# Performance work log

Hardware: AMD Instinct MI355X
Metric: run time of the kernel (lower is better)

The kernel has to match this reference:

```python
import jax, jax.numpy as jnp
import numpy as np

N_NODES = 50000
N_EDGES = 800000
D_IN = 512
D_OUT = 256

def setup_inputs() -> dict:
    key = jax.random.key(0)
    k1, k2, k3, k4, k5 = jax.random.split(key, 5)
    return {
        "inputs": jax.random.normal(k1, (N_NODES, D_IN), dtype=jnp.float32),
        "weights": jax.random.uniform(k2, (D_IN, D_OUT), dtype=jnp.float32, minval=-0.1, maxval=0.1),
        "bias": jnp.zeros((D_OUT,), dtype=jnp.float32),
        "edge_vals": jax.random.uniform(k3, (N_EDGES,), dtype=jnp.float32),
        "edge_row": jax.random.randint(k4, (N_EDGES,), 0, N_NODES),
        "edge_col": jax.random.randint(k5, (N_EDGES,), 0, N_NODES),
    }

def reference(inputs, weights, bias, edge_vals, edge_row, edge_col):
    # dense projection: [N, D_in] @ [D_in, D_out] -> [N, D_out]
    supports = inputs @ weights
    # sparse adjacency spmm in COO form: out[i] = sum_e vals[e] * supports[col[e]] for row[e] == i
    msgs = supports[edge_col] * edge_vals[:, None]  # [E, D_out]
    aggregated = jax.ops.segment_sum(msgs, edge_row, num_segments=inputs.shape[0])
    return aggregated + bias
```

## Files before the change

### kernel.cpp

```cpp
#include <hip/hip_runtime.h>

#define D_IN 512
#define D_OUT 256
#define BM 128
#define BN 128
#define BK 32
#define LDK 40

typedef short short8 __attribute__((ext_vector_type(8)));
typedef float floatx4 __attribute__((ext_vector_type(4)));

static __device__ __forceinline__ unsigned short f2bf(float f) {
    unsigned u = __float_as_uint(f);
    u += 0x7FFF + ((u >> 16) & 1);
    return (unsigned short)(u >> 16);
}
static __device__ __forceinline__ float bf2f(unsigned short h) {
    return __uint_as_float((unsigned)h << 16);
}

__global__ __launch_bounds__(256) void convert_w(const float* __restrict__ W,
                                                 unsigned short* __restrict__ Wt) {
    int t = blockIdx.x * 256 + threadIdx.x;
    int n = t >> 9;
    int k = t & 511;
    Wt[t] = f2bf(W[(size_t)k * D_OUT + n]);
}

__global__ __launch_bounds__(512) void gemm_bf16(const float* __restrict__ A,
                                                 const unsigned short* __restrict__ Wt,
                                                 unsigned short* __restrict__ S, int M) {
    __shared__ unsigned short As[BM * LDK];
    __shared__ unsigned short Bs[BN * LDK];
    const int tid  = threadIdx.x;
    const int lane = tid & 63;
    const int wave = tid >> 6;
    const int wm   = (wave >> 2) * 64;
    const int wn   = (wave & 3) * 32;
    const int bm   = blockIdx.x * BM;
    const int bn   = blockIdx.y * BN;
    const int l15  = lane & 15;
    const int quad = lane >> 4;

    const float* aptr[2];
    const unsigned short* bptr[2];
    int aoff[2], boff[2];
    bool aval[2];
#pragma unroll
    for (int i = 0; i < 2; ++i) {
        int item = tid + i * 512;
        int m  = item >> 3;
        int k4 = (item & 7) * 4;
        int gm = bm + m;
        aval[i] = gm < M;
        aptr[i] = A + (size_t)(aval[i] ? gm : 0) * D_IN + k4;
        aoff[i] = m * LDK + k4;
        bptr[i] = Wt + (size_t)(bn + m) * D_IN + k4;
        boff[i] = m * LDK + k4;
    }

    float4  aR[2];
    ushort4 bR[2];
#pragma unroll
    for (int i = 0; i < 2; ++i) {
        aR[i] = aval[i] ? *(const float4*)(aptr[i]) : make_float4(0.f, 0.f, 0.f, 0.f);
        bR[i] = *(const ushort4*)(bptr[i]);
    }

    floatx4 acc[4][2] = {};

    for (int k0 = 0; k0 < D_IN; k0 += BK) {
#pragma unroll
        for (int i = 0; i < 2; ++i) {
            ushort4 b;
            b.x = f2bf(aR[i].x); b.y = f2bf(aR[i].y);
            b.z = f2bf(aR[i].z); b.w = f2bf(aR[i].w);
            *(ushort4*)(As + aoff[i]) = b;
            *(ushort4*)(Bs + boff[i]) = bR[i];
        }
        __syncthreads();

        if (k0 + BK < D_IN) {
#pragma unroll
            for (int i = 0; i < 2; ++i) {
                aR[i] = aval[i] ? *(const float4*)(aptr[i] + k0 + BK)
                                : make_float4(0.f, 0.f, 0.f, 0.f);
                bR[i] = *(const ushort4*)(bptr[i] + k0 + BK);
            }
        }

        short8 af[4], bfr[2];
#pragma unroll
        for (int i = 0; i < 4; ++i)
            af[i] = *(const short8*)(As + (wm + i * 16 + l15) * LDK + quad * 8);
#pragma unroll
        for (int j = 0; j < 2; ++j)
            bfr[j] = *(const short8*)(Bs + (wn + j * 16 + l15) * LDK + quad * 8);
#pragma unroll
        for (int i = 0; i < 4; ++i)
#pragma unroll
            for (int j = 0; j < 2; ++j)
                acc[i][j] = __builtin_amdgcn_mfma_f32_16x16x32_bf16(
                    af[i], bfr[j], acc[i][j], 0, 0, 0);
        __syncthreads();
    }

#pragma unroll
    for (int i = 0; i < 4; ++i) {
#pragma unroll
        for (int r = 0; r < 4; ++r) {
            int gm = bm + wm + i * 16 + quad * 4 + r;
            if (gm < M) {
#pragma unroll
                for (int j = 0; j < 2; ++j)
                    S[(size_t)gm * D_OUT + bn + wn + j * 16 + l15] = f2bf(acc[i][j][r]);
            }
        }
    }
}

__global__ __launch_bounds__(256) void hist_rows(const int* __restrict__ rows,
                                                 int* __restrict__ cnt, int E) {
    int e = blockIdx.x * 256 + threadIdx.x;
    if (e < E) atomicAdd(&cnt[rows[e]], 1);
}

#define SCAN_B 4096
__global__ __launch_bounds__(1024) void scan_blocks(const int* __restrict__ cnt,
                                                    int* __restrict__ ptr,
                                                    int* __restrict__ partials, int M) {
    __shared__ int wsum[16];
    const int t = threadIdx.x, lane = t & 63, wave = t >> 6;
    const int base = blockIdx.x * SCAN_B + t * 4;
    int4 v = make_int4(0, 0, 0, 0);
    if (base + 3 < M) v = *(const int4*)(cnt + base);
    else {
        if (base + 0 < M) v.x = cnt[base + 0];
        if (base + 1 < M) v.y = cnt[base + 1];
        if (base + 2 < M) v.z = cnt[base + 2];
        if (base + 3 < M) v.w = cnt[base + 3];
    }
    int s = v.x + v.y + v.z + v.w;
    int incl = s;
#pragma unroll
    for (int off = 1; off < 64; off <<= 1) {
        int x = __shfl_up(incl, off, 64);
        if (lane >= off) incl += x;
    }
    if (lane == 63) wsum[wave] = incl;
    __syncthreads();
    if (t == 0) {
        int run = 0;
#pragma unroll
        for (int w = 0; w < 16; ++w) { int x = wsum[w]; wsum[w] = run; run += x; }
        partials[blockIdx.x] = run;
    }
    __syncthreads();
    int e0 = wsum[wave] + (incl - s);
    int e1 = e0 + v.x, e2 = e1 + v.y, e3 = e2 + v.z;
    if (base + 3 < M) *(int4*)(ptr + base) = make_int4(e0, e1, e2, e3);
    else {
        if (base + 0 < M) ptr[base + 0] = e0;
        if (base + 1 < M) ptr[base + 1] = e1;
        if (base + 2 < M) ptr[base + 2] = e2;
        if (base + 3 < M) ptr[base + 3] = e3;
    }
}

__global__ __launch_bounds__(64) void scan_partials(int* __restrict__ partials,
                                                    int* __restrict__ ptr, int M, int nb) {
    const int t = threadIdx.x;
    int v = (t < nb) ? partials[t] : 0;
    int incl = v;
#pragma unroll
    for (int off = 1; off < 64; off <<= 1) {
        int x = __shfl_up(incl, off, 64);
        if (t >= off) incl += x;
    }
    if (t < nb) partials[t] = incl - v;
    if (t == 63) ptr[M] = incl;
}

__global__ __launch_bounds__(256) void add_offsets(int* __restrict__ ptr,
                                                   const int* __restrict__ partials,
                                                   int M) {
    int i = blockIdx.x * 256 + threadIdx.x;
    if (i < M) ptr[i] += partials[i >> 12];
}

__global__ __launch_bounds__(256) void build_sorted(const float* __restrict__ vals,
                                                    const int* __restrict__ rows,
                                                    const int* __restrict__ cols,
                                                    const int* __restrict__ ptr,
                                                    int* __restrict__ cnt,
                                                    int2* __restrict__ edges, int E) {
    int e = blockIdx.x * 256 + threadIdx.x;
    if (e >= E) return;
    int r = rows[e];
    int pos = ptr[r] + atomicAdd(&cnt[r], 1);
    edges[pos] = make_int2(cols[e], __float_as_int(vals[e]));
}

__global__ __launch_bounds__(256) void spmm_rows(const unsigned short* __restrict__ S,
                                                 const int2* __restrict__ edges,
                                                 const int* __restrict__ ptr,
                                                 const float* __restrict__ bias,
                                                 float* __restrict__ out, int M) {
    const int row = blockIdx.x * 4 + (threadIdx.x >> 6);
    if (row >= M) return;
    const int lane = threadIdx.x & 63;
    float4 a0 = ((const float4*)bias)[lane];
    float4 a1 = make_float4(0.f, 0.f, 0.f, 0.f);
    const int beg = ptr[row];
    const int end = ptr[row + 1];
    int j = beg;
    for (; j + 3 < end; j += 4) {
        int2 e0 = edges[j], e1 = edges[j + 1], e2 = edges[j + 2], e3 = edges[j + 3];
        ushort4 s0 = ((const ushort4*)(S + (size_t)e0.x * D_OUT))[lane];
        ushort4 s1 = ((const ushort4*)(S + (size_t)e1.x * D_OUT))[lane];
        ushort4 s2 = ((const ushort4*)(S + (size_t)e2.x * D_OUT))[lane];
        ushort4 s3 = ((const ushort4*)(S + (size_t)e3.x * D_OUT))[lane];
        float v0 = __int_as_float(e0.y), v1 = __int_as_float(e1.y);
        float v2 = __int_as_float(e2.y), v3 = __int_as_float(e3.y);
        a0.x += v0 * bf2f(s0.x) + v2 * bf2f(s2.x);
        a0.y += v0 * bf2f(s0.y) + v2 * bf2f(s2.y);
        a0.z += v0 * bf2f(s0.z) + v2 * bf2f(s2.z);
        a0.w += v0 * bf2f(s0.w) + v2 * bf2f(s2.w);
        a1.x += v1 * bf2f(s1.x) + v3 * bf2f(s3.x);
        a1.y += v1 * bf2f(s1.y) + v3 * bf2f(s3.y);
        a1.z += v1 * bf2f(s1.z) + v3 * bf2f(s3.z);
        a1.w += v1 * bf2f(s1.w) + v3 * bf2f(s3.w);
    }
    for (; j < end; ++j) {
        int2 e = edges[j];
        float v = __int_as_float(e.y);
        ushort4 s = ((const ushort4*)(S + (size_t)e.x * D_OUT))[lane];
        a0.x += v * bf2f(s.x);
        a0.y += v * bf2f(s.y);
        a0.z += v * bf2f(s.z);
        a0.w += v * bf2f(s.w);
    }
    a0.x += a1.x; a0.y += a1.y; a0.z += a1.z; a0.w += a1.w;
    ((float4*)out)[(size_t)row * 64 + lane] = a0;
}

extern "C" void kernel_launch(void* const* d_in, const int* in_sizes, int n_in,
                              void* d_out, int out_size, void* d_ws, size_t ws_size,
                              hipStream_t stream) {
    const float* inputs    = (const float*)d_in[0];
    const float* weights   = (const float*)d_in[1];
    const float* bias      = (const float*)d_in[2];
    const float* edge_vals = (const float*)d_in[3];
    const int*   edge_row  = (const int*)d_in[4];
    const int*   edge_col  = (const int*)d_in[5];
    float* out = (float*)d_out;

    const int M = in_sizes[0] / D_IN;
    const int E = in_sizes[3];

    char* ws = (char*)d_ws;
    unsigned short* S  = (unsigned short*)ws;
    unsigned short* Wt = (unsigned short*)(ws + (size_t)M * D_OUT * 2);
    int2* edges        = (int2*)((char*)Wt + (size_t)D_OUT * D_IN * 2);
    int*  ptr          = (int*)((char*)edges + (size_t)E * 8);
    int*  cnt          = ptr + ((M + 4) & ~3);
    int*  partials     = cnt + M;

    convert_w<<<(D_IN * D_OUT) / 256, 256, 0, stream>>>(weights, Wt);

    dim3 ggrid((M + BM - 1) / BM, D_OUT / BN);
    gemm_bf16<<<ggrid, 512, 0, stream>>>(inputs, Wt, S, M);

    hipMemsetAsync(cnt, 0, (size_t)M * 4, stream);
    hist_rows<<<(E + 255) / 256, 256, 0, stream>>>(edge_row, cnt, E);
    int nb = (M + SCAN_B - 1) / SCAN_B;
    scan_blocks<<<nb, 1024, 0, stream>>>(cnt, ptr, partials, M);
    scan_partials<<<1, 64, 0, stream>>>(partials, ptr, M, nb);
    add_offsets<<<(M + 255) / 256, 256, 0, stream>>>(ptr, partials, M);
    hipMemsetAsync(cnt, 0, (size_t)M * 4, stream);
    build_sorted<<<(E + 255) / 256, 256, 0, stream>>>(edge_vals, edge_row, edge_col,
                                                      ptr, cnt, edges, E);

    spmm_rows<<<(M + 3) / 4, 256, 0, stream>>>(S, edges, ptr, bias, out, M);
}
```

Measured before the change: 335.7 us.

## Fuse GEMM with edge bucketing, merge weight conversion with count zeroing

Merges weight conversion and count zeroing into one launch, dropping two memsets. The edge-bucketing pass now runs as extra blocks of the GEMM launch, so the two can overlap. Bucketing uses atomicAdd on ptr directly, removing the second count array; spmm then reads row bounds shifted by one. The GEMM tile becomes 64 rows by the full 256 columns, so each A tile is loaded once; spmm gets an 8-way unroll and nontemporal output stores. The fused launch raises register and shared-memory pressure and mixes two very different kinds of blocks.

```diff
diff --git a/kernel.cpp b/kernel.cpp
--- a/kernel.cpp
+++ b/kernel.cpp
@@ -2,8 +2,7 @@
 
 #define D_IN 512
 #define D_OUT 256
-#define BM 128
-#define BN 128
+#define BM 64
 #define BK 32
 #define LDK 40
 
@@ -19,103 +18,19 @@
     return __uint_as_float((unsigned)h << 16);
 }
 
-__global__ __launch_bounds__(256) void convert_w(const float* __restrict__ W,
-                                                 unsigned short* __restrict__ Wt) {
-    int t = blockIdx.x * 256 + threadIdx.x;
-    int n = t >> 9;
-    int k = t & 511;
-    Wt[t] = f2bf(W[(size_t)k * D_OUT + n]);
-}
-
-__global__ __launch_bounds__(512) void gemm_bf16(const float* __restrict__ A,
-                                                 const unsigned short* __restrict__ Wt,
-                                                 unsigned short* __restrict__ S, int M) {
-    __shared__ unsigned short As[BM * LDK];
-    __shared__ unsigned short Bs[BN * LDK];
-    const int tid  = threadIdx.x;
-    const int lane = tid & 63;
-    const int wave = tid >> 6;
-    const int wm   = (wave >> 2) * 64;
-    const int wn   = (wave & 3) * 32;
-    const int bm   = blockIdx.x * BM;
-    const int bn   = blockIdx.y * BN;
-    const int l15  = lane & 15;
-    const int quad = lane >> 4;
-
-    const float* aptr[2];
-    const unsigned short* bptr[2];
-    int aoff[2], boff[2];
-    bool aval[2];
-#pragma unroll
-    for (int i = 0; i < 2; ++i) {
-        int item = tid + i * 512;
-        int m  = item >> 3;
-        int k4 = (item & 7) * 4;
-        int gm = bm + m;
-        aval[i] = gm < M;
-        aptr[i] = A + (size_t)(aval[i] ? gm : 0) * D_IN + k4;
-        aoff[i] = m * LDK + k4;
-        bptr[i] = Wt + (size_t)(bn + m) * D_IN + k4;
-        boff[i] = m * LDK + k4;
-    }
-
-    float4  aR[2];
-    ushort4 bR[2];
-#pragma unroll
-    for (int i = 0; i < 2; ++i) {
-        aR[i] = aval[i] ? *(const float4*)(aptr[i]) : make_float4(0.f, 0.f, 0.f, 0.f);
-        bR[i] = *(const ushort4*)(bptr[i]);
-    }
-
-    floatx4 acc[4][2] = {};
-
-    for (int k0 = 0; k0 < D_IN; k0 += BK) {
-#pragma unroll
-        for (int i = 0; i < 2; ++i) {
-            ushort4 b;
-            b.x = f2bf(aR[i].x); b.y = f2bf(aR[i].y);
-            b.z = f2bf(aR[i].z); b.w = f2bf(aR[i].w);
-            *(ushort4*)(As + aoff[i]) = b;
-            *(ushort4*)(Bs + boff[i]) = bR[i];
-        }
-        __syncthreads();
-
-        if (k0 + BK < D_IN) {
-#pragma unroll
-            for (int i = 0; i < 2; ++i) {
-                aR[i] = aval[i] ? *(const float4*)(aptr[i] + k0 + BK)
-                                : make_float4(0.f, 0.f, 0.f, 0.f);
-                bR[i] = *(const ushort4*)(bptr[i] + k0 + BK);
-            }
-        }
-
-        short8 af[4], bfr[2];
-#pragma unroll
-        for (int i = 0; i < 4; ++i)
-            af[i] = *(const short8*)(As + (wm + i * 16 + l15) * LDK + quad * 8);
-#pragma unroll
-        for (int j = 0; j < 2; ++j)
-            bfr[j] = *(const short8*)(Bs + (wn + j * 16 + l15) * LDK + quad * 8);
-#pragma unroll
-        for (int i = 0; i < 4; ++i)
-#pragma unroll
-            for (int j = 0; j < 2; ++j)
-                acc[i][j] = __builtin_amdgcn_mfma_f32_16x16x32_bf16(
-                    af[i], bfr[j], acc[i][j], 0, 0, 0);
-        __syncthreads();
-    }
-
-#pragma unroll
-    for (int i = 0; i < 4; ++i) {
-#pragma unroll
-        for (int r = 0; r < 4; ++r) {
-            int gm = bm + wm + i * 16 + quad * 4 + r;
-            if (gm < M) {
-#pragma unroll
-                for (int j = 0; j < 2; ++j)
-                    S[(size_t)gm * D_OUT + bn + wn + j * 16 + l15] = f2bf(acc[i][j][r]);
-            }
-        }
+#define CONV_BLOCKS 256
+__global__ __launch_bounds__(512) void convert_and_zero(const float* __restrict__ W,
+                                                        unsigned short* __restrict__ Wt,
+                                                        int* __restrict__ cnt, int M) {
+    int b = blockIdx.x;
+    if (b < CONV_BLOCKS) {
+        int t = b * 512 + threadIdx.x;
+        int n = t >> 9;
+        int k = t & 511;
+        Wt[t] = f2bf(W[(size_t)k * D_OUT + n]);
+    } else {
+        int i = (b - CONV_BLOCKS) * 512 + threadIdx.x;
+        if (i < M) cnt[i] = 0;
     }
 }
 
@@ -188,17 +103,100 @@
     if (i < M) ptr[i] += partials[i >> 12];
 }
 
-__global__ __launch_bounds__(256) void build_sorted(const float* __restrict__ vals,
-                                                    const int* __restrict__ rows,
-                                                    const int* __restrict__ cols,
-                                                    const int* __restrict__ ptr,
-                                                    int* __restrict__ cnt,
-                                                    int2* __restrict__ edges, int E) {
-    int e = blockIdx.x * 256 + threadIdx.x;
-    if (e >= E) return;
-    int r = rows[e];
-    int pos = ptr[r] + atomicAdd(&cnt[r], 1);
-    edges[pos] = make_int2(cols[e], __float_as_int(vals[e]));
+__global__ __launch_bounds__(512, 4) void gemm_build(
+    const float* __restrict__ A, const unsigned short* __restrict__ Wt,
+    unsigned short* __restrict__ S, int M, int nGemm,
+    const float* __restrict__ vals, const int* __restrict__ rows,
+    const int* __restrict__ cols, int* __restrict__ ptr,
+    int2* __restrict__ edges, int E) {
+    __shared__ unsigned short As[BM * LDK];
+    __shared__ unsigned short Bs[D_OUT * LDK];
+    const int tid = threadIdx.x;
+
+    if ((int)blockIdx.x >= nGemm) {
+        int e = ((int)blockIdx.x - nGemm) * 512 + tid;
+        if (e < E) {
+            int r = rows[e];
+            int pos = atomicAdd(&ptr[r], 1);
+            edges[pos] = make_int2(cols[e], __float_as_int(vals[e]));
+        }
+        return;
+    }
+
+    const int lane = tid & 63;
+    const int wave = tid >> 6;
+    const int wn   = wave * 32;
+    const int bm   = blockIdx.x * BM;
+    const int l15  = lane & 15;
+    const int quad = lane >> 4;
+
+    const int am   = tid >> 3;
+    const int ak4  = (tid & 7) * 4;
+    const bool aval = (bm + am) < M;
+    const float* aptr = A + (size_t)(aval ? bm + am : 0) * D_IN + ak4;
+    const int aoff = am * LDK + ak4;
+
+    const unsigned short* bptr[2];
+    int boff[2];
+#pragma unroll
+    for (int i = 0; i < 2; ++i) {
+        int item = tid + i * 512;
+        int bn = item >> 2;
+        int k8 = (item & 3) * 8;
+        bptr[i] = Wt + (size_t)bn * D_IN + k8;
+        boff[i] = bn * LDK + k8;
+    }
+
+    float4 aR = aval ? *(const float4*)aptr : make_float4(0.f, 0.f, 0.f, 0.f);
+    short8 bR[2];
+#pragma unroll
+    for (int i = 0; i < 2; ++i) bR[i] = *(const short8*)(bptr[i]);
+
+    floatx4 acc[4][2] = {};
+
+    for (int k0 = 0; k0 < D_IN; k0 += BK) {
+        ushort4 ab;
+        ab.x = f2bf(aR.x); ab.y = f2bf(aR.y); ab.z = f2bf(aR.z); ab.w = f2bf(aR.w);
+        *(ushort4*)(As + aoff) = ab;
+#pragma unroll
+        for (int i = 0; i < 2; ++i) *(short8*)(Bs + boff[i]) = bR[i];
+        __syncthreads();
+
+        if (k0 + BK < D_IN) {
+            aR = aval ? *(const float4*)(aptr + k0 + BK)
+                      : make_float4(0.f, 0.f, 0.f, 0.f);
+#pragma unroll
+            for (int i = 0; i < 2; ++i) bR[i] = *(const short8*)(bptr[i] + k0 + BK);
+        }
+
+        short8 af[4], bfr[2];
+#pragma unroll
+        for (int i = 0; i < 4; ++i)
+            af[i] = *(const short8*)(As + (i * 16 + l15) * LDK + quad * 8);
+#pragma unroll
+        for (int j = 0; j < 2; ++j)
+            bfr[j] = *(const short8*)(Bs + (wn + j * 16 + l15) * LDK + quad * 8);
+#pragma unroll
+        for (int i = 0; i < 4; ++i)
+#pragma unroll
+            for (int j = 0; j < 2; ++j)
+                acc[i][j] = __builtin_amdgcn_mfma_f32_16x16x32_bf16(
+                    af[i], bfr[j], acc[i][j], 0, 0, 0);
+        __syncthreads();
+    }
+
+#pragma unroll
+    for (int i = 0; i < 4; ++i) {
+#pragma unroll
+        for (int r = 0; r < 4; ++r) {
+            int gm = bm + i * 16 + quad * 4 + r;
+            if (gm < M) {
+#pragma unroll
+                for (int j = 0; j < 2; ++j)
+                    S[(size_t)gm * D_OUT + wn + j * 16 + l15] = f2bf(acc[i][j][r]);
+            }
+        }
+    }
 }
 
 __global__ __launch_bounds__(256) void spmm_rows(const unsigned short* __restrict__ S,
@@ -211,9 +209,33 @@
     const int lane = threadIdx.x & 63;
     float4 a0 = ((const float4*)bias)[lane];
     float4 a1 = make_float4(0.f, 0.f, 0.f, 0.f);
-    const int beg = ptr[row];
-    const int end = ptr[row + 1];
+    const int beg = row ? ptr[row - 1] : 0;
+    const int end = ptr[row];
     int j = beg;
+    for (; j + 7 < end; j += 8) {
+        int2 e0 = edges[j + 0], e1 = edges[j + 1], e2 = edges[j + 2], e3 = edges[j + 3];
+        int2 e4 = edges[j + 4], e5 = edges[j + 5], e6 = edges[j + 6], e7 = edges[j + 7];
+        ushort4 s0 = ((const ushort4*)(S + (size_t)e0.x * D_OUT))[lane];
+        ushort4 s1 = ((const ushort4*)(S + (size_t)e1.x * D_OUT))[lane];
+        ushort4 s2 = ((const ushort4*)(S + (size_t)e2.x * D_OUT))[lane];
+        ushort4 s3 = ((const ushort4*)(S + (size_t)e3.x * D_OUT))[lane];
+        ushort4 s4 = ((const ushort4*)(S + (size_t)e4.x * D_OUT))[lane];
+        ushort4 s5 = ((const ushort4*)(S + (size_t)e5.x * D_OUT))[lane];
+        ushort4 s6 = ((const ushort4*)(S + (size_t)e6.x * D_OUT))[lane];
+        ushort4 s7 = ((const ushort4*)(S + (size_t)e7.x * D_OUT))[lane];
+        float v0 = __int_as_float(e0.y), v1 = __int_as_float(e1.y);
+        float v2 = __int_as_float(e2.y), v3 = __int_as_float(e3.y);
+        float v4 = __int_as_float(e4.y), v5 = __int_as_float(e5.y);
+        float v6 = __int_as_float(e6.y), v7 = __int_as_float(e7.y);
+        a0.x += v0 * bf2f(s0.x) + v2 * bf2f(s2.x) + v4 * bf2f(s4.x) + v6 * bf2f(s6.x);
+        a0.y += v0 * bf2f(s0.y) + v2 * bf2f(s2.y) + v4 * bf2f(s4.y) + v6 * bf2f(s6.y);
+        a0.z += v0 * bf2f(s0.z) + v2 * bf2f(s2.z) + v4 * bf2f(s4.z) + v6 * bf2f(s6.z);
+        a0.w += v0 * bf2f(s0.w) + v2 * bf2f(s2.w) + v4 * bf2f(s4.w) + v6 * bf2f(s6.w);
+        a1.x += v1 * bf2f(s1.x) + v3 * bf2f(s3.x) + v5 * bf2f(s5.x) + v7 * bf2f(s7.x);
+        a1.y += v1 * bf2f(s1.y) + v3 * bf2f(s3.y) + v5 * bf2f(s5.y) + v7 * bf2f(s7.y);
+        a1.z += v1 * bf2f(s1.z) + v3 * bf2f(s3.z) + v5 * bf2f(s5.z) + v7 * bf2f(s7.z);
+        a1.w += v1 * bf2f(s1.w) + v3 * bf2f(s3.w) + v5 * bf2f(s5.w) + v7 * bf2f(s7.w);
+    }
     for (; j + 3 < end; j += 4) {
         int2 e0 = edges[j], e1 = edges[j + 1], e2 = edges[j + 2], e3 = edges[j + 3];
         ushort4 s0 = ((const ushort4*)(S + (size_t)e0.x * D_OUT))[lane];
@@ -241,7 +263,8 @@
         a0.w += v * bf2f(s.w);
     }
     a0.x += a1.x; a0.y += a1.y; a0.z += a1.z; a0.w += a1.w;
-    ((float4*)out)[(size_t)row * 64 + lane] = a0;
+    floatx4 res = {a0.x, a0.y, a0.z, a0.w};
+    __builtin_nontemporal_store(res, (floatx4*)(out + (size_t)row * D_OUT) + lane);
 }
 
 extern "C" void kernel_launch(void* const* d_in, const int* in_sizes, int n_in,
@@ -266,20 +289,20 @@
     int*  cnt          = ptr + ((M + 4) & ~3);
     int*  partials     = cnt + M;
 
-    convert_w<<<(D_IN * D_OUT) / 256, 256, 0, stream>>>(weights, Wt);
-
-    dim3 ggrid((M + BM - 1) / BM, D_OUT / BN);
-    gemm_bf16<<<ggrid, 512, 0, stream>>>(inputs, Wt, S, M);
-
-    hipMemsetAsync(cnt, 0, (size_t)M * 4, stream);
+    int nzero = (M + 511) / 512;
+    convert_and_zero<<<CONV_BLOCKS + nzero, 512, 0, stream>>>(weights, Wt, cnt, M);
+
     hist_rows<<<(E + 255) / 256, 256, 0, stream>>>(edge_row, cnt, E);
     int nb = (M + SCAN_B - 1) / SCAN_B;
     scan_blocks<<<nb, 1024, 0, stream>>>(cnt, ptr, partials, M);
     scan_partials<<<1, 64, 0, stream>>>(partials, ptr, M, nb);
     add_offsets<<<(M + 255) / 256, 256, 0, stream>>>(ptr, partials, M);
-    hipMemsetAsync(cnt, 0, (size_t)M * 4, stream);
-    build_sorted<<<(E + 255) / 256, 256, 0, stream>>>(edge_vals, edge_row, edge_col,
-                                                      ptr, cnt, edges, E);
+
+    int nGemm  = (M + BM - 1) / BM;
+    int nBuild = (E + 511) / 512;
+    gemm_build<<<nGemm + nBuild, 512, 0, stream>>>(inputs, Wt, S, M, nGemm,
+                                                   edge_vals, edge_row, edge_col,
+                                                   ptr, edges, E);
 
     spmm_rows<<<(M + 3) / 4, 256, 0, stream>>>(S, edges, ptr, bias, out, M);
 }
```

Result: faster. 311.1 us (-7.3%).
